# Performance work log

Measured on AMD Instinct MI355X. Metric: run time of the kernel, lower is better.

Reference implementation:

```python
import jax, jax.numpy as jnp
import numpy as np

N_NODES = 50000
N_EDGES = 800000
IN_DIM = 3
OUT_DIM = 50


def _glorot(key, shape):
    fan_in, fan_out = shape[0], shape[1]
    lim = np.sqrt(6.0 / (fan_in + fan_out))
    return jax.random.uniform(key, shape, jnp.float32, -lim, lim)


def setup_inputs() -> dict:
    key = jax.random.key(0)
    ks = jax.random.split(key, 16)
    x = jax.random.normal(ks[0], (N_NODES, IN_DIM), jnp.float32)
    edge_index = jax.random.randint(ks[1], (2, N_EDGES), 0, N_NODES, jnp.int64)
    return {
        "x": x,
        "edge_index": edge_index,
        # pointwise Conv1d (kernel_size=1) == per-node Linear; store as [in, out]
        "w1": _glorot(ks[2], (IN_DIM, 32)), "b1": jnp.zeros((32,), jnp.float32),
        "w2": _glorot(ks[3], (32, 64)),     "b2": jnp.zeros((64,), jnp.float32),
        "w3": _glorot(ks[4], (64, 128)),    "b3": jnp.zeros((128,), jnp.float32),
        # GCNConv weights [in, out] + bias
        "g1w": _glorot(ks[5], (128, 256)),  "g1b": jnp.zeros((256,), jnp.float32),
        "g2w": _glorot(ks[6], (256, 512)),  "g2b": jnp.zeros((512,), jnp.float32),
        "g3w": _glorot(ks[7], (512, OUT_DIM)), "g3b": jnp.zeros((OUT_DIM,), jnp.float32),
    }


def _gcn_conv(h, src, dst, dinv, W, b):
    """PyG GCNConv: add self-loops + symmetric norm. h: [N, Fin]."""
    n = h.shape[0]
    h = h @ W  # [N, Fout]
    norm = dinv[src] * dinv[dst]  # [E]
    msg = h[src] * norm[:, None]  # gather over edges [E, Fout]
    agg = jax.ops.segment_sum(msg, dst, num_segments=n)
    # self-loop contribution: norm = dinv[i]^2
    agg = agg + h * (dinv * dinv)[:, None]
    return agg + b


def reference(x, edge_index, w1, b1, w2, b2, w3, b3, g1w, g1b, g2w, g2b, g3w, g3b):
    src, dst = edge_index[0], edge_index[1]
    n = x.shape[0]
    # degree with self-loops (in-degree on targets), shared by all GCN layers
    deg = jnp.zeros((n,), x.dtype).at[dst].add(1.0) + 1.0
    dinv = jax.lax.rsqrt(deg)

    # pointwise conv stack (1x1 Conv1d == per-node dense layer)
    h = jax.nn.relu(x @ w1 + b1)
    h = jax.nn.relu(h @ w2 + b2)
    h = jax.nn.relu(h @ w3 + b3)

    h = jax.nn.relu(_gcn_conv(h, src, dst, dinv, g1w, g1b))
    h = jax.nn.relu(_gcn_conv(h, src, dst, dinv, g2w, g2b))
    h = _gcn_conv(h, src, dst, dinv, g3w, g3b)
    return jax.nn.softmax(h, axis=1)  # [N, OUT_DIM]
```

## Files before the change

### kernel.cpp

```cpp
#include <hip/hip_runtime.h>
#include <hip/hip_bf16.h>
#include <math.h>


typedef __attribute__((ext_vector_type(8))) short short8;
typedef __attribute__((ext_vector_type(8))) _Float16 half8;
typedef __attribute__((ext_vector_type(4))) float floatx4;

__device__ __forceinline__ unsigned short bf16h(float f) {
    unsigned int u = __float_as_uint(f);
    u += 0x7fff + ((u >> 16) & 1);
    return (unsigned short)(u >> 16);
}
__device__ __forceinline__ float bf16f(unsigned short h) {
    return __uint_as_float(((unsigned int)h) << 16);
}

__device__ __forceinline__ void gld_lds16(unsigned short* lds, const unsigned short* g) {
    __builtin_amdgcn_global_load_lds(
        (const __attribute__((address_space(1))) unsigned int*)g,
        (__attribute__((address_space(3))) unsigned int*)lds, 16, 0, 0);
}


__global__ void hist_kernel(const int* __restrict__ dst, int* __restrict__ counts, int e) {
    int g = blockIdx.x * blockDim.x + threadIdx.x;
    if (g < e) atomicAdd(&counts[dst[g]], 1);
}

__global__ void scan1_kernel(const int* __restrict__ counts, int* __restrict__ bsum, int n) {
    __shared__ int buf[256];
    int i = blockIdx.x * 256 + threadIdx.x;
    buf[threadIdx.x] = (i < n) ? counts[i] : 0;
    __syncthreads();
    for (int off = 128; off > 0; off >>= 1) {
        if (threadIdx.x < off) buf[threadIdx.x] += buf[threadIdx.x + off];
        __syncthreads();
    }
    if (threadIdx.x == 0) bsum[blockIdx.x] = buf[0];
}

__global__ void scan2_kernel(const int* __restrict__ bsum, int* __restrict__ bsumx,
                             int* __restrict__ offsets, int nb, int n) {
    __shared__ int buf[256];
    int tid = threadIdx.x;
    int v = (tid < nb) ? bsum[tid] : 0;
    buf[tid] = v;
    __syncthreads();
    for (int off = 1; off < 256; off <<= 1) {
        int t = (tid >= off) ? buf[tid - off] : 0;
        __syncthreads();
        buf[tid] += t;
        __syncthreads();
    }
    if (tid < nb) bsumx[tid] = buf[tid] - v;
    if (tid == 255) offsets[n] = buf[255];
}

__global__ void scan3_kernel(const int* __restrict__ counts, const int* __restrict__ bsumx,
                             int* __restrict__ offsets, int* __restrict__ cursor,
                             float* __restrict__ dinv, int n) {
    __shared__ int buf[256];
    int tid = threadIdx.x;
    int i = blockIdx.x * 256 + tid;
    int c = (i < n) ? counts[i] : 0;
    buf[tid] = c;
    __syncthreads();
    for (int off = 1; off < 256; off <<= 1) {
        int t = (tid >= off) ? buf[tid - off] : 0;
        __syncthreads();
        buf[tid] += t;
        __syncthreads();
    }
    if (i < n) {
        int excl = bsumx[blockIdx.x] + buf[tid] - c;
        offsets[i] = excl;
        cursor[i] = excl;
        dinv[i] = rsqrtf((float)c + 1.0f);
    }
}

__global__ void fill_kernel(const int* __restrict__ src, const int* __restrict__ dst,
                            const float* __restrict__ dinv, int* __restrict__ cursor,
                            int* __restrict__ ssrc, float* __restrict__ snorm, int e) {
    int g = blockIdx.x * blockDim.x + threadIdx.x;
    if (g >= e) return;
    int s = src[g], d = dst[g];
    int pos = atomicAdd(&cursor[d], 1);
    ssrc[pos]  = s;
    snorm[pos] = dinv[s] * dinv[d];
}


__device__ __forceinline__ void wsplit_one(float w, unsigned short* Bt, int k, int n, int K) {
    unsigned short h = bf16h(w);
    unsigned short l = bf16h(w - bf16f(h));
    size_t base = (size_t)n * (2 * K);
    Bt[base + k]     = h;
    Bt[base + K + k] = l;
}

__global__ void prepw_kernel(const float* __restrict__ g1w, const float* __restrict__ g2w,
                             const float* __restrict__ g3w, const float* __restrict__ w3,
                             unsigned short* __restrict__ Bt1,
                             unsigned short* __restrict__ Bt2,
                             unsigned short* __restrict__ Bt3,
                             unsigned short* __restrict__ Bt0) {
    int gid = blockIdx.x * blockDim.x + threadIdx.x;
    if (gid < 32768) {
        int k = gid >> 8, n = gid & 255;
        wsplit_one(g1w[gid], Bt1, k, n, 128);
    } else if (gid < 32768 + 131072) {
        int idx = gid - 32768;
        int k = idx >> 9, n = idx & 511;
        wsplit_one(g2w[idx], Bt2, k, n, 256);
    } else if (gid < 32768 + 131072 + 32768) {
        int idx = gid - 32768 - 131072;
        int k = idx >> 6, c = idx & 63;
        float w = (c < 50) ? g3w[k * 50 + c] : 0.0f;
        wsplit_one(w, Bt3, k, c, 512);
    } else if (gid < 32768 + 131072 + 32768 + 8192) {
        int idx = gid - 32768 - 131072 - 32768;
        int k = idx >> 7, n = idx & 127;
        wsplit_one(w3[idx], Bt0, k, n, 64);
    }
}


__global__ __launch_bounds__(256) void mlp12_kernel(
        const float* __restrict__ x,
        const float* __restrict__ w1, const float* __restrict__ b1,
        const float* __restrict__ w2, const float* __restrict__ b2,
        unsigned short* __restrict__ H2h, unsigned short* __restrict__ H2l, int n) {
    __shared__ float sw1[96], sb1[32], sw2[2048], sb2[64];
    int tid = threadIdx.x;
    if (tid < 96) sw1[tid] = w1[tid];
    if (tid < 32) sb1[tid] = b1[tid];
    if (tid < 64) sb2[tid] = b2[tid];
    for (int i = tid; i < 2048; i += 256) sw2[i] = w2[i];
    __syncthreads();

    int node = blockIdx.x * 256 + tid;
    if (node >= n) return;
    float x0 = x[node * 3 + 0], x1 = x[node * 3 + 1], x2 = x[node * 3 + 2];
    float h1[32];
#pragma unroll
    for (int j = 0; j < 32; j++)
        h1[j] = fmaxf(sb1[j] + x0 * sw1[j] + x1 * sw1[32 + j] + x2 * sw1[64 + j], 0.0f);

    float acc[64];
#pragma unroll
    for (int j = 0; j < 64; j++) acc[j] = sb2[j];
    for (int k = 0; k < 32; k++) {
        float hk = h1[k];
#pragma unroll
        for (int j4 = 0; j4 < 16; j4++) {
            float4 w = *(const float4*)&sw2[k * 64 + j4 * 4];
            acc[j4 * 4 + 0] = fmaf(hk, w.x, acc[j4 * 4 + 0]);
            acc[j4 * 4 + 1] = fmaf(hk, w.y, acc[j4 * 4 + 1]);
            acc[j4 * 4 + 2] = fmaf(hk, w.z, acc[j4 * 4 + 2]);
            acc[j4 * 4 + 3] = fmaf(hk, w.w, acc[j4 * 4 + 3]);
        }
    }
#pragma unroll
    for (int j4 = 0; j4 < 16; j4++) {
        ushort4 h4, l4;
        unsigned short* hp = (unsigned short*)&h4;
        unsigned short* lp = (unsigned short*)&l4;
#pragma unroll
        for (int t = 0; t < 4; t++) {
            float v = fmaxf(acc[j4 * 4 + t], 0.0f);
            unsigned short h = bf16h(v);
            hp[t] = h;
            lp[t] = bf16h(v - bf16f(h));
        }
        *(ushort4*)&H2h[(size_t)node * 64 + j4 * 4] = h4;
        *(ushort4*)&H2l[(size_t)node * 64 + j4 * 4] = l4;
    }
}


template<int BM, int BN, int WAVES, int WGR, int WGC, int WRF, int WCF, int MODE, bool AF16>
__global__ __launch_bounds__(WAVES * 64) void gemm_mfma_kernel(
        const unsigned short* __restrict__ Ah, const unsigned short* __restrict__ Al,
        const unsigned short* __restrict__ Bt, const float* __restrict__ bias,
        float* __restrict__ Cf, unsigned short* __restrict__ Ch,
        unsigned short* __restrict__ Cl, int M, int K, int N) {
    static_assert(WGR * WRF * 16 == BM, "row cover");
    static_assert(WGC * WCF * 16 == BN, "col cover");
    static_assert(WGR * WGC == WAVES, "wave grid");
    constexpr int AUNITS = AF16 ? (BM / 16) : (BM / 8);
    constexpr int BUNITS = BN / 8;
    static_assert(AUNITS % WAVES == 0 && BUNITS % WAVES == 0, "staging split");
    __shared__ __align__(16) unsigned short Ash[BM * 32];
    __shared__ __align__(16) unsigned short Asl[AF16 ? 16 : BM * 32];
    __shared__ __align__(16) unsigned short Bsh[BN * 32];
    __shared__ __align__(16) unsigned short Bsl[BN * 32];

    const int tid  = threadIdx.x;
    const int lane = tid & 63;
    const int wave = tid >> 6;
    const int bm = blockIdx.y * BM;
    const int bn = blockIdx.x * BN;
    const int K2 = 2 * K;

    const int wr0 = (wave / WGC) * (WRF * 16);
    const int wc0 = (wave % WGC) * (WCF * 16);
    const int lr   = lane & 15;
    const int quad = lane >> 4;
    const int arow = lane >> 2;
    const int acol = (lane & 3) * 8;

    floatx4 acc[WRF][WCF];
#pragma unroll
    for (int i = 0; i < WRF; i++)
#pragma unroll
        for (int j = 0; j < WCF; j++) acc[i][j] = floatx4{0.f, 0.f, 0.f, 0.f};

    for (int k0 = 0; k0 < K; k0 += 32) {
#pragma unroll
        for (int u = 0; u < AUNITS / WAVES; u++) {
            int unit = wave + u * WAVES;
            if (AF16) {
                int grp = unit;
                int gm = bm + grp * 16 + arow;
                if (gm >= M) gm = M - 1;
                gld_lds16(&Ash[grp * 512], Ah + (size_t)gm * K + k0 + acol);
            } else {
                int grp = unit >> 1, pl = unit & 1;
                int gm = bm + grp * 16 + arow;
                if (gm >= M) gm = M - 1;
                size_t go = (size_t)gm * K + k0 + acol;
                if (pl) gld_lds16(&Asl[grp * 512], Al + go);
                else    gld_lds16(&Ash[grp * 512], Ah + go);
            }
        }
#pragma unroll
        for (int u = 0; u < BUNITS / WAVES; u++) {
            int unit = wave + u * WAVES;
            int grp = unit >> 1, pl = unit & 1;
            int gr = bn + grp * 16 + arow;
            size_t go = (size_t)gr * K2 + k0 + acol + (pl ? K : 0);
            if (pl) gld_lds16(&Bsl[grp * 512], Bt + go);
            else    gld_lds16(&Bsh[grp * 512], Bt + go);
        }
        __syncthreads();

        short8 ahf[WRF], alf[WRF], bhf[WCF], blf[WCF];
#pragma unroll
        for (int i = 0; i < WRF; i++) {
            int ro = (wr0 + i * 16 + lr) * 32 + quad * 8;
            if (AF16) {
                half8 av = *reinterpret_cast<const half8*>(&Ash[ro]);
#pragma unroll
                for (int t = 0; t < 8; t++) {
                    float f = (float)av[t];
                    unsigned short h = bf16h(f);
                    ahf[i][t] = (short)h;
                    alf[i][t] = (short)bf16h(f - bf16f(h));
                }
            } else {
                ahf[i] = *reinterpret_cast<const short8*>(&Ash[ro]);
                alf[i] = *reinterpret_cast<const short8*>(&Asl[ro]);
            }
        }
#pragma unroll
        for (int j = 0; j < WCF; j++) {
            int ro = (wc0 + j * 16 + lr) * 32 + quad * 8;
            bhf[j] = *reinterpret_cast<const short8*>(&Bsh[ro]);
            blf[j] = *reinterpret_cast<const short8*>(&Bsl[ro]);
        }
#pragma unroll
        for (int i = 0; i < WRF; i++)
#pragma unroll
            for (int j = 0; j < WCF; j++) {
                acc[i][j] = __builtin_amdgcn_mfma_f32_16x16x32_bf16(
                    ahf[i], bhf[j], acc[i][j], 0, 0, 0);
                acc[i][j] = __builtin_amdgcn_mfma_f32_16x16x32_bf16(
                    ahf[i], blf[j], acc[i][j], 0, 0, 0);
                acc[i][j] = __builtin_amdgcn_mfma_f32_16x16x32_bf16(
                    alf[i], bhf[j], acc[i][j], 0, 0, 0);
            }
        __syncthreads();
    }

#pragma unroll
    for (int i = 0; i < WRF; i++) {
#pragma unroll
        for (int j = 0; j < WCF; j++) {
            int gc = bn + wc0 + j * 16 + lr;
#pragma unroll
            for (int reg = 0; reg < 4; reg++) {
                int gr = bm + wr0 + i * 16 + quad * 4 + reg;
                if (gr >= M) continue;
                float v = acc[i][j][reg];
                if (MODE == 0) {
                    v = fmaxf(v + bias[gc], 0.0f);
                    Cf[(size_t)gr * N + gc] = v;
                } else if (MODE == 1) {
                    v = fmaxf(v + bias[gc], 0.0f);
                    unsigned short h = bf16h(v);
                    unsigned short l = bf16h(v - bf16f(h));
                    Ch[(size_t)gr * N + gc] = h;
                    Cl[(size_t)gr * N + gc] = l;
                } else if (MODE == 2) {
                    Cf[(size_t)gr * N + gc] = v;
                } else if (MODE == 3) {
                    v = fmaxf(v + bias[gc], 0.0f);
                    ((_Float16*)Ch)[(size_t)gr * N + gc] = (_Float16)v;
                } else {
                    ((_Float16*)Ch)[(size_t)gr * N + gc] = (_Float16)v;
                }
            }
        }
    }
}


template<int F>
__global__ void agg_f16_kernel(const _Float16* __restrict__ table,
                               const int* __restrict__ offsets,
                               const int* __restrict__ ssrc,
                               const float* __restrict__ snorm,
                               const float* __restrict__ dinv,
                               unsigned short* __restrict__ Ah,
                               unsigned short* __restrict__ Al, int n) {
    constexpr int F8 = F / 8;
    int gid = blockIdx.x * blockDim.x + threadIdx.x;
    if (gid >= n * F8) return;
    int node = gid / F8;
    int c8 = (gid - node * F8) * 8;

    float acc[8];
#pragma unroll
    for (int i = 0; i < 8; i++) acc[i] = 0.0f;

    int beg = offsets[node], end = offsets[node + 1];
    for (int e = beg; e < end; ++e) {
        int s = ssrc[e];
        float w = snorm[e];
        half8 r = *reinterpret_cast<const half8*>(table + (size_t)s * F + c8);
#pragma unroll
        for (int i = 0; i < 8; i++) acc[i] = fmaf((float)r[i], w, acc[i]);
    }
    float dv = dinv[node];
    float sw = dv * dv;
    half8 r = *reinterpret_cast<const half8*>(table + (size_t)node * F + c8);
#pragma unroll
    for (int i = 0; i < 8; i++) acc[i] = fmaf((float)r[i], sw, acc[i]);

    unsigned short hb[8], lb[8];
#pragma unroll
    for (int i = 0; i < 8; i++) {
        unsigned short h = bf16h(acc[i]);
        hb[i] = h;
        lb[i] = bf16h(acc[i] - bf16f(h));
    }
    *(uint4*)&Ah[(size_t)node * F + c8] = *(uint4*)hb;
    *(uint4*)&Al[(size_t)node * F + c8] = *(uint4*)lb;
}


__global__ void agg50_softmax_kernel(const _Float16* __restrict__ z,
                                     const int* __restrict__ offsets,
                                     const int* __restrict__ ssrc,
                                     const float* __restrict__ snorm,
                                     const float* __restrict__ dinv,
                                     const float* __restrict__ bias,
                                     float* __restrict__ out, int n) {
    int node = blockIdx.x * 4 + (threadIdx.x >> 6);
    int lane = threadIdx.x & 63;
    if (node >= n) return;

    float a0 = 0.f, a1 = 0.f, a2 = 0.f, a3 = 0.f;
    int beg = offsets[node], end = offsets[node + 1];
    int e = beg;
    for (; e + 4 <= end; e += 4) {
        int s0 = ssrc[e + 0], s1 = ssrc[e + 1], s2 = ssrc[e + 2], s3 = ssrc[e + 3];
        float w0 = snorm[e + 0], w1 = snorm[e + 1];
        float w2 = snorm[e + 2], w3 = snorm[e + 3];
        float r0 = (float)z[(size_t)s0 * 64 + lane];
        float r1 = (float)z[(size_t)s1 * 64 + lane];
        float r2 = (float)z[(size_t)s2 * 64 + lane];
        float r3 = (float)z[(size_t)s3 * 64 + lane];
        a0 = fmaf(r0, w0, a0);
        a1 = fmaf(r1, w1, a1);
        a2 = fmaf(r2, w2, a2);
        a3 = fmaf(r3, w3, a3);
    }
    for (; e < end; ++e)
        a0 = fmaf((float)z[(size_t)ssrc[e] * 64 + lane], snorm[e], a0);

    float dv = dinv[node];
    float a = fmaf((float)z[(size_t)node * 64 + lane], dv * dv,
                   (a0 + a1) + (a2 + a3));

    float v = (lane < 50) ? a + bias[lane] : -INFINITY;
    float m = v;
#pragma unroll
    for (int off = 32; off > 0; off >>= 1) m = fmaxf(m, __shfl_xor(m, off));
    float ex = (lane < 50) ? expf(v - m) : 0.0f;
    float s = ex;
#pragma unroll
    for (int off = 32; off > 0; off >>= 1) s += __shfl_xor(s, off);
    if (lane < 50) out[(size_t)node * 50 + lane] = ex / s;
}


extern "C" void kernel_launch(void* const* d_in, const int* in_sizes, int n_in,
                              void* d_out, int out_size, void* d_ws, size_t ws_size,
                              hipStream_t stream) {
    const float* x    = (const float*)d_in[0];
    const int*   ei   = (const int*)  d_in[1];
    const float* w1   = (const float*)d_in[2];
    const float* b1   = (const float*)d_in[3];
    const float* w2   = (const float*)d_in[4];
    const float* b2   = (const float*)d_in[5];
    const float* w3   = (const float*)d_in[6];
    const float* b3   = (const float*)d_in[7];
    const float* g1w  = (const float*)d_in[8];
    const float* g1b  = (const float*)d_in[9];
    const float* g2w  = (const float*)d_in[10];
    const float* g2b  = (const float*)d_in[11];
    const float* g3w  = (const float*)d_in[12];
    const float* g3b  = (const float*)d_in[13];
    float* out = (float*)d_out;

    const int N = in_sizes[0] / 3;
    const int E = in_sizes[1] / 2;
    const int* src = ei;
    const int* dst = ei + E;
    const int NB = (N + 255) / 256;

    char* ws = (char*)d_ws;
    size_t off = 0;
    auto alloc = [&](size_t bytes) -> char* {
        char* p = ws + off;
        off = (off + bytes + 255) & ~(size_t)255;
        return p;
    };
    int*   counts  = (int*)  alloc((size_t)N * 4);
    int*   offsets = (int*)  alloc((size_t)(N + 1) * 4);
    int*   cursor  = (int*)  alloc((size_t)N * 4);
    float* dinv    = (float*)alloc((size_t)N * 4);
    int*   bsum    = (int*)  alloc((size_t)256 * 4);
    int*   bsumx   = (int*)  alloc((size_t)256 * 4);
    int*   ssrc    = (int*)  alloc((size_t)E * 4);
    float* snorm   = (float*)alloc((size_t)E * 4);
    unsigned short* Bt1 = (unsigned short*)alloc((size_t)256 * 256 * 2);
    unsigned short* Bt2 = (unsigned short*)alloc((size_t)512 * 512 * 2);
    unsigned short* Bt3 = (unsigned short*)alloc((size_t)64 * 1024 * 2);
    unsigned short* Bt0 = (unsigned short*)alloc((size_t)128 * 128 * 2);
    char* R1 = alloc((size_t)N * 256 * 4);
    char* R2 = alloc((size_t)N * 256 * 4);
    char* R3 = alloc((size_t)N * 512 * 2);
    (void)ws_size;

    _Float16*       S128f = (_Float16*)R1;
    unsigned short* A128h = (unsigned short*)(R1 + (size_t)N * 128 * 2);
    unsigned short* A128l = (unsigned short*)(R1 + (size_t)N * 128 * 4);
    unsigned short* A256h = (unsigned short*)R1;
    unsigned short* A256l = (unsigned short*)(R1 + (size_t)N * 256 * 2);
    unsigned short* H2h  = (unsigned short*)R2;
    unsigned short* H2l  = (unsigned short*)(R2 + (size_t)N * 64 * 2);
    _Float16*       G1f  = (_Float16*)R2;
    _Float16*       zbuf = (_Float16*)R2;
    _Float16*       A512f = (_Float16*)R3;

    hipMemsetAsync(counts, 0, (size_t)N * 4, stream);
    hist_kernel<<<(E + 255) / 256, 256, 0, stream>>>(dst, counts, E);
    scan1_kernel<<<NB, 256, 0, stream>>>(counts, bsum, N);
    scan2_kernel<<<1, 256, 0, stream>>>(bsum, bsumx, offsets, NB, N);
    scan3_kernel<<<NB, 256, 0, stream>>>(counts, bsumx, offsets, cursor, dinv, N);
    fill_kernel<<<(E + 255) / 256, 256, 0, stream>>>(src, dst, dinv, cursor, ssrc, snorm, E);
    prepw_kernel<<<(204800 + 255) / 256, 256, 0, stream>>>(
        g1w, g2w, g3w, w3, Bt1, Bt2, Bt3, Bt0);

    const int MB = (N + 127) / 128;
    const int MB64 = (N + 63) / 64;

    mlp12_kernel<<<NB, 256, 0, stream>>>(x, w1, b1, w2, b2, H2h, H2l, N);
    {   dim3 grid(1, MB);
        gemm_mfma_kernel<128, 128, 4, 2, 2, 4, 4, 3, false><<<grid, 256, 0, stream>>>(
            H2h, H2l, Bt0, b3, nullptr, (unsigned short*)S128f, nullptr, N, 64, 128);
    }

    agg_f16_kernel<128><<<((size_t)N * 16 + 255) / 256, 256, 0, stream>>>(
        S128f, offsets, ssrc, snorm, dinv, A128h, A128l, N);
    {   dim3 grid(2, MB);
        gemm_mfma_kernel<128, 128, 4, 2, 2, 4, 4, 3, false><<<grid, 256, 0, stream>>>(
            A128h, A128l, Bt1, g1b, nullptr, (unsigned short*)G1f, nullptr, N, 128, 256);
    }

    agg_f16_kernel<256><<<((size_t)N * 32 + 255) / 256, 256, 0, stream>>>(
        G1f, offsets, ssrc, snorm, dinv, A256h, A256l, N);
    {   dim3 grid(4, MB);
        gemm_mfma_kernel<128, 128, 4, 2, 2, 4, 4, 3, false><<<grid, 256, 0, stream>>>(
            A256h, A256l, Bt2, g2b, nullptr, (unsigned short*)A512f, nullptr, N, 256, 512);
    }

    {   dim3 grid(1, MB64);
        gemm_mfma_kernel<64, 64, 4, 4, 1, 1, 4, 4, true><<<grid, 256, 0, stream>>>(
            (const unsigned short*)A512f, nullptr, Bt3, nullptr,
            nullptr, (unsigned short*)zbuf, nullptr, N, 512, 64);
    }
    agg50_softmax_kernel<<<(N + 3) / 4, 256, 0, stream>>>(
        zbuf, offsets, ssrc, snorm, dinv, g3b, out, N);
}
```

Measured before the change: 489.7 us.

## Store aggregated features as fp16 and swizzle GEMM block order for reuse

```diff
diff --git a/kernel.cpp b/kernel.cpp
--- a/kernel.cpp
+++ b/kernel.cpp
@@ -180,7 +180,8 @@
 }
 
 
-template<int BM, int BN, int WAVES, int WGR, int WGC, int WRF, int WCF, int MODE, bool AF16>
+template<int BM, int BN, int WAVES, int WGR, int WGC, int WRF, int WCF, int MODE,
+         bool AF16, int SWIZCOLS>
 __global__ __launch_bounds__(WAVES * 64) void gemm_mfma_kernel(
         const unsigned short* __restrict__ Ah, const unsigned short* __restrict__ Al,
         const unsigned short* __restrict__ Bt, const float* __restrict__ bias,
@@ -197,11 +198,23 @@
     __shared__ __align__(16) unsigned short Bsh[BN * 32];
     __shared__ __align__(16) unsigned short Bsl[BN * 32];
 
+    int bm, bn;
+    if (SWIZCOLS > 0) {
+        constexpr int CSH = (SWIZCOLS == 4) ? 2 : 1;
+        int b = blockIdx.x;
+        int col = (b >> 3) & (SWIZCOLS - 1);
+        int row = ((b >> (3 + CSH)) << 3) | (b & 7);
+        bm = row * BM;
+        bn = col * BN;
+        if (bm >= M) return;
+    } else {
+        bm = blockIdx.y * BM;
+        bn = blockIdx.x * BN;
+    }
+
     const int tid  = threadIdx.x;
     const int lane = tid & 63;
     const int wave = tid >> 6;
-    const int bm = blockIdx.y * BM;
-    const int bn = blockIdx.x * BN;
     const int K2 = 2 * K;
 
     const int wr0 = (wave / WGC) * (WRF * 16);
@@ -323,8 +336,7 @@
                                const int* __restrict__ ssrc,
                                const float* __restrict__ snorm,
                                const float* __restrict__ dinv,
-                               unsigned short* __restrict__ Ah,
-                               unsigned short* __restrict__ Al, int n) {
+                               _Float16* __restrict__ Aout, int n) {
     constexpr int F8 = F / 8;
     int gid = blockIdx.x * blockDim.x + threadIdx.x;
     if (gid >= n * F8) return;
@@ -349,15 +361,10 @@
 #pragma unroll
     for (int i = 0; i < 8; i++) acc[i] = fmaf((float)r[i], sw, acc[i]);
 
-    unsigned short hb[8], lb[8];
-#pragma unroll
-    for (int i = 0; i < 8; i++) {
-        unsigned short h = bf16h(acc[i]);
-        hb[i] = h;
-        lb[i] = bf16h(acc[i] - bf16f(h));
-    }
-    *(uint4*)&Ah[(size_t)node * F + c8] = *(uint4*)hb;
-    *(uint4*)&Al[(size_t)node * F + c8] = *(uint4*)lb;
+    half8 o;
+#pragma unroll
+    for (int i = 0; i < 8; i++) o[i] = (_Float16)acc[i];
+    *reinterpret_cast<half8*>(&Aout[(size_t)node * F + c8]) = o;
 }
 
 
@@ -457,10 +464,8 @@
     (void)ws_size;
 
     _Float16*       S128f = (_Float16*)R1;
-    unsigned short* A128h = (unsigned short*)(R1 + (size_t)N * 128 * 2);
-    unsigned short* A128l = (unsigned short*)(R1 + (size_t)N * 128 * 4);
-    unsigned short* A256h = (unsigned short*)R1;
-    unsigned short* A256l = (unsigned short*)(R1 + (size_t)N * 256 * 2);
+    _Float16*       A128f = (_Float16*)(R1 + (size_t)N * 128 * 2);
+    _Float16*       A256f = (_Float16*)R1;
     unsigned short* H2h  = (unsigned short*)R2;
     unsigned short* H2l  = (unsigned short*)(R2 + (size_t)N * 64 * 2);
     _Float16*       G1f  = (_Float16*)R2;
@@ -477,30 +482,33 @@
         g1w, g2w, g3w, w3, Bt1, Bt2, Bt3, Bt0);
 
     const int MB = (N + 127) / 128;
+    const int MB8 = (MB + 7) & ~7;
     const int MB64 = (N + 63) / 64;
 
     mlp12_kernel<<<NB, 256, 0, stream>>>(x, w1, b1, w2, b2, H2h, H2l, N);
     {   dim3 grid(1, MB);
-        gemm_mfma_kernel<128, 128, 4, 2, 2, 4, 4, 3, false><<<grid, 256, 0, stream>>>(
+        gemm_mfma_kernel<128, 128, 4, 2, 2, 4, 4, 3, false, 0><<<grid, 256, 0, stream>>>(
             H2h, H2l, Bt0, b3, nullptr, (unsigned short*)S128f, nullptr, N, 64, 128);
     }
 
     agg_f16_kernel<128><<<((size_t)N * 16 + 255) / 256, 256, 0, stream>>>(
-        S128f, offsets, ssrc, snorm, dinv, A128h, A128l, N);
-    {   dim3 grid(2, MB);
-        gemm_mfma_kernel<128, 128, 4, 2, 2, 4, 4, 3, false><<<grid, 256, 0, stream>>>(
-            A128h, A128l, Bt1, g1b, nullptr, (unsigned short*)G1f, nullptr, N, 128, 256);
+        S128f, offsets, ssrc, snorm, dinv, A128f, N);
+    {
+        gemm_mfma_kernel<128, 128, 4, 2, 2, 4, 4, 3, true, 2><<<2 * MB8, 256, 0, stream>>>(
+            (const unsigned short*)A128f, nullptr, Bt1, g1b,
+            nullptr, (unsigned short*)G1f, nullptr, N, 128, 256);
     }
 
     agg_f16_kernel<256><<<((size_t)N * 32 + 255) / 256, 256, 0, stream>>>(
-        G1f, offsets, ssrc, snorm, dinv, A256h, A256l, N);
-    {   dim3 grid(4, MB);
-        gemm_mfma_kernel<128, 128, 4, 2, 2, 4, 4, 3, false><<<grid, 256, 0, stream>>>(
-            A256h, A256l, Bt2, g2b, nullptr, (unsigned short*)A512f, nullptr, N, 256, 512);
+        G1f, offsets, ssrc, snorm, dinv, A256f, N);
+    {
+        gemm_mfma_kernel<128, 128, 4, 2, 2, 4, 4, 3, true, 4><<<4 * MB8, 256, 0, stream>>>(
+            (const unsigned short*)A256f, nullptr, Bt2, g2b,
+            nullptr, (unsigned short*)A512f, nullptr, N, 256, 512);
     }
 
     {   dim3 grid(1, MB64);
-        gemm_mfma_kernel<64, 64, 4, 4, 1, 1, 4, 4, true><<<grid, 256, 0, stream>>>(
+        gemm_mfma_kernel<64, 64, 4, 4, 1, 1, 4, 4, true, 0><<<grid, 256, 0, stream>>>(
             (const unsigned short*)A512f, nullptr, Bt3, nullptr,
             nullptr, (unsigned short*)zbuf, nullptr, N, 512, 64);
     }
```

New measurement: 489.6 us. About the same (-0.0%).
